# Kernel tuning notes

Hardware: AMD Instinct MI355X
Metric: run time of the kernel (lower is better)

Reference implementation:

```python
import jax, jax.numpy as jnp
import numpy as np

N_NODES, N_EDGES, D_IN, D_OUT = 50000, 400000, 512, 512


def setup_inputs() -> dict:
    key = jax.random.key(0)
    k = jax.random.split(key, 7)
    s = 1.0 / np.sqrt(D_IN)
    return {
        "x": jax.random.normal(k[0], (N_NODES, D_IN), dtype=jnp.float32),
        "src": jax.random.randint(k[1], (N_EDGES,), 0, N_NODES),
        "dst": jax.random.randint(k[2], (N_EDGES,), 0, N_NODES),
        "W1": jax.random.uniform(k[3], (D_IN, D_OUT), jnp.float32, -s, s),
        "b1": jax.random.uniform(k[4], (D_OUT,), jnp.float32, -s, s),
        "W2": jax.random.uniform(k[5], (D_IN, D_OUT), jnp.float32, -s, s),
        "b2": jax.random.uniform(k[6], (D_OUT,), jnp.float32, -s, s),
    }


def reference(x, src, dst, W1, b1, W2, b2):
    n_nodes = x.shape[0]
    # gather src features along each edge, segment-sum into dst nodes
    msg_sum = jax.ops.segment_sum(x[src], dst, num_segments=n_nodes)      # [N, D_in]
    counts = jax.ops.segment_sum(jnp.ones_like(dst, dtype=x.dtype), dst,
                                 num_segments=n_nodes)                    # [N]
    mean = msg_sum / jnp.maximum(counts, 1.0)[:, None]                    # mailbox mean
    out = (x @ W1 + b1) + ((x - mean) @ W2 + b2)
    # DGL update_all leaves nodes with no incoming messages untouched
    return jnp.where((counts > 0)[:, None], out, x)
```

## Files before the change

### kernel.cpp

```cpp
#include <hip/hip_runtime.h>
#include <hip/hip_bf16.h>
#include <stdint.h>

typedef unsigned short u16;
typedef unsigned int   u32;

#define N_NODES 50000
#define N_EDGES 400000
#define DDIM    512
#define KTOT    1024
#define BM      256
#define BMS     256
#define BN      256
#define BK      32
#define NT      (KTOT / BK)
#define MTILES  ((N_NODES + BM - 1) / BM)
#define NTILES  (DDIM / BN)
#define NWG     (MTILES * NTILES)

typedef __attribute__((ext_vector_type(8))) __bf16 bf16x8;
typedef __attribute__((ext_vector_type(4))) float  f32x4;

#define S_VMCNT(n) do { asm volatile("s_waitcnt vmcnt(" #n ")" ::: "memory"); \
                        __builtin_amdgcn_sched_barrier(0); } while (0)
#define S_LGKM0()  do { asm volatile("s_waitcnt lgkmcnt(0)" ::: "memory"); \
                        __builtin_amdgcn_sched_barrier(0); } while (0)

__device__ __forceinline__ float bflo(u32 d) { return __builtin_bit_cast(float, d << 16); }
__device__ __forceinline__ float bfhi(u32 d) { return __builtin_bit_cast(float, d & 0xffff0000u); }
__device__ __forceinline__ u16 f2bf(float f) {
    u32 u = __builtin_bit_cast(u32, f);
    u32 r = u + 0x7fffu + ((u >> 16) & 1u);
    return (u16)(r >> 16);
}
__device__ __forceinline__ u32 pack2(float a, float b) {
    return (u32)f2bf(a) | ((u32)f2bf(b) << 16);
}
__device__ __forceinline__ void gload_lds16(const void* g, void* l) {
    __builtin_amdgcn_global_load_lds(
        (const __attribute__((address_space(1))) void*)g,
        (__attribute__((address_space(3))) void*)l, 16, 0, 0);
}

__global__ void cvt_k(const float* __restrict__ x, u16* __restrict__ Acat) {
    int i = blockIdx.x * 256 + threadIdx.x;
    int node = i >> 6, c8 = i & 63;
    const float4* p = (const float4*)(x + (size_t)node * DDIM + c8 * 8);
    float4 a = p[0], b = p[1];
    uint4 o;
    o.x = pack2(a.x, a.y); o.y = pack2(a.z, a.w);
    o.z = pack2(b.x, b.y); o.w = pack2(b.z, b.w);
    *(uint4*)(Acat + (size_t)node * KTOT + c8 * 8) = o;
}

__global__ void hist_k(const int* __restrict__ dst, int* __restrict__ counts) {
    int e = blockIdx.x * 256 + threadIdx.x;
    if (e < N_EDGES) atomicAdd(&counts[dst[e]], 1);
}

#define NCHUNK 49
__global__ __launch_bounds__(1024) void scanA_k(const int* __restrict__ counts, int* __restrict__ csum) {
    __shared__ int ws[16];
    int t = threadIdx.x, b = blockIdx.x;
    int i = b * 1024 + t;
    int v = (i < N_NODES) ? counts[i] : 0;
    for (int d = 32; d; d >>= 1) v += __shfl_down(v, d);
    if ((t & 63) == 0) ws[t >> 6] = v;
    __syncthreads();
    if (t < 16) {
        int s = ws[t];
        for (int d = 8; d; d >>= 1) s += __shfl_down(s, d);
        if (t == 0) csum[b] = s;
    }
}
__global__ void scanB_k(int* __restrict__ csum) {
    int t = threadIdx.x;
    int v = (t < NCHUNK) ? csum[t] : 0;
    int s = v;
    for (int d = 1; d < 64; d <<= 1) { int u = __shfl_up(s, d); if (t >= d) s += u; }
    if (t < NCHUNK) csum[t] = s - v;
}
__global__ __launch_bounds__(1024) void scanC_k(const int* __restrict__ counts, const int* __restrict__ csum,
                                                int* __restrict__ offsets, int* __restrict__ cursor) {
    __shared__ int wsum[16];
    int t = threadIdx.x, b = blockIdx.x;
    int i = b * 1024 + t;
    int lane = t & 63, w = t >> 6;
    int v = (i < N_NODES) ? counts[i] : 0;
    int s = v;
    for (int d = 1; d < 64; d <<= 1) { int u = __shfl_up(s, d); if (lane >= d) s += u; }
    if (lane == 63) wsum[w] = s;
    __syncthreads();
    if (t < 16) {
        int ww = wsum[t], ss = ww;
        for (int d = 1; d < 16; d <<= 1) { int u = __shfl_up(ss, d); if (t >= d) ss += u; }
        wsum[t] = ss - ww;
    }
    __syncthreads();
    int excl = (s - v) + wsum[w] + csum[b];
    if (i < N_NODES) { offsets[i] = excl; cursor[i] = excl; }
}

__global__ void fill_k(const int* __restrict__ src, const int* __restrict__ dst,
                       int* __restrict__ cursor, int* __restrict__ esrc) {
    int e = blockIdx.x * 256 + threadIdx.x;
    if (e < N_EDGES) {
        int d = dst[e];
        int p = atomicAdd(&cursor[d], 1);
        esrc[p] = src[e];
    }
}

__global__ void prepw_k(const float* __restrict__ W1, const float* __restrict__ W2,
                        const float* __restrict__ b1, const float* __restrict__ b2,
                        u16* __restrict__ Wcat, float* __restrict__ b12) {
    int idx = blockIdx.x * 256 + threadIdx.x;
    int k = idx >> 9, n = idx & 511;
    float w1 = W1[idx], w2 = W2[idx];
    Wcat[(size_t)n * KTOT + k]       = f2bf(w1 + w2);
    Wcat[(size_t)n * KTOT + 512 + k] = f2bf(w2);
    if (idx < 512) b12[idx] = b1[idx] + b2[idx];
}

__device__ __forceinline__ void addrow(float* acc, uint4 v) {
    acc[0] += bflo(v.x); acc[1] += bfhi(v.x);
    acc[2] += bflo(v.y); acc[3] += bfhi(v.y);
    acc[4] += bflo(v.z); acc[5] += bfhi(v.z);
    acc[6] += bflo(v.w); acc[7] += bfhi(v.w);
}
__global__ __launch_bounds__(256) void agg_k(u16* Acat,
                                             const int* __restrict__ offsets,
                                             const int* __restrict__ counts,
                                             const int* __restrict__ esrc) {
    int nid = blockIdx.x * 4 + (threadIdx.x >> 6);
    if (nid >= N_NODES) return;
    int lane = threadIdx.x & 63;
    int off = offsets[nid], deg = counts[nid];
    float acc[8] = {0, 0, 0, 0, 0, 0, 0, 0};
    int e = 0;
    for (; e + 7 < deg; e += 8) {
        int s[8];
        #pragma unroll
        for (int u = 0; u < 8; u++) s[u] = esrc[off + e + u];
        uint4 v[8];
        #pragma unroll
        for (int u = 0; u < 8; u++)
            v[u] = *(const uint4*)(Acat + (size_t)s[u] * KTOT + lane * 8);
        #pragma unroll
        for (int u = 0; u < 8; u++) addrow(acc, v[u]);
    }
    for (; e + 3 < deg; e += 4) {
        int s0 = esrc[off + e], s1 = esrc[off + e + 1];
        int s2 = esrc[off + e + 2], s3 = esrc[off + e + 3];
        uint4 v0 = *(const uint4*)(Acat + (size_t)s0 * KTOT + lane * 8);
        uint4 v1 = *(const uint4*)(Acat + (size_t)s1 * KTOT + lane * 8);
        uint4 v2 = *(const uint4*)(Acat + (size_t)s2 * KTOT + lane * 8);
        uint4 v3 = *(const uint4*)(Acat + (size_t)s3 * KTOT + lane * 8);
        addrow(acc, v0); addrow(acc, v1); addrow(acc, v2); addrow(acc, v3);
    }
    for (; e < deg; e++) {
        int s0 = esrc[off + e];
        addrow(acc, *(const uint4*)(Acat + (size_t)s0 * KTOT + lane * 8));
    }
    float scale = (deg > 0) ? (-1.0f / (float)deg) : 0.0f;
    uint4 o;
    o.x = pack2(acc[0] * scale, acc[1] * scale);
    o.y = pack2(acc[2] * scale, acc[3] * scale);
    o.z = pack2(acc[4] * scale, acc[5] * scale);
    o.w = pack2(acc[6] * scale, acc[7] * scale);
    *(uint4*)(Acat + (size_t)nid * KTOT + 512 + lane * 8) = o;
}

__global__ __launch_bounds__(512, 2) void gemm_k(const u16* __restrict__ Acat,
                                                 const float* __restrict__ x,
                                                 const u16* __restrict__ Wcat,
                                                 const float* __restrict__ b12,
                                                 const int* __restrict__ counts,
                                                 float* __restrict__ out) {
    __shared__ u16 As[4][BMS * BK];
    __shared__ u16 Bs[4][BN * BK];

    const int tlin = (blockIdx.x & 7) * (NWG / 8) + (blockIdx.x >> 3);
    const int m0 = (tlin >> 1) * BM;
    const int n0 = (tlin & 1) * BN;

    const int tid  = threadIdx.x;
    const int lane = tid & 63;
    const int wid  = tid >> 6;
    const int wm = wid >> 2, wn = wid & 3;
    const int quad = lane >> 4, lr = lane & 15;

    const int rloc  = tid >> 2;
    const int koffu = (((tid & 3) ^ ((tid >> 3) & 3)) << 3);
    int arow[2], brow[2];
    #pragma unroll
    for (int q = 0; q < 2; q++) {
        int r = m0 + q * 128 + rloc;
        arow[q] = (r < N_NODES) ? r : (N_NODES - 1);
        brow[q] = n0 + q * 128 + rloc;
    }

    auto stage = [&](int t) {
        u16* A_c = &As[t & 3][0]; u16* B_c = &Bs[t & 3][0];
        const int k0 = t * BK;
        #pragma unroll
        for (int q = 0; q < 2; q++)
            gload_lds16(Acat + (size_t)arow[q] * KTOT + k0 + koffu,
                        A_c + q * 4096 + wid * 512);
        #pragma unroll
        for (int q = 0; q < 2; q++)
            gload_lds16(Wcat + (size_t)brow[q] * KTOT + k0 + koffu,
                        B_c + q * 4096 + wid * 512);
    };

    const int rswb = ((lr >> 1) & 3) << 4;
    auto ldA = [&](const u16* A_c, int mf) -> bf16x8 {
        int row = wm * 128 + mf * 16 + lr;
        return *(const bf16x8*)((const char*)A_c + row * 64 + ((quad << 4) ^ rswb));
    };
    auto ldB = [&](const u16* B_c, int nf) -> bf16x8 {
        int row = wn * 64 + nf * 16 + lr;
        return *(const bf16x8*)((const char*)B_c + row * 64 + ((quad << 4) ^ rswb));
    };

    f32x4 acc[8][4] = {};

    stage(0); stage(1); stage(2);
    S_VMCNT(8);
    __builtin_amdgcn_s_barrier();

    #pragma unroll 1
    for (int t = 0; t < NT; ++t) {
        const u16* A_c = &As[t & 3][0];
        const u16* B_c = &Bs[t & 3][0];

        bf16x8 af[8], bf[4];
        #pragma unroll
        for (int i = 0; i < 8; i++) af[i] = ldA(A_c, i);
        #pragma unroll
        for (int j = 0; j < 4; j++) bf[j] = ldB(B_c, j);

        if (t + 3 < NT) stage(t + 3);

        __builtin_amdgcn_s_setprio(1);
        #pragma unroll
        for (int i = 0; i < 8; i++)
            #pragma unroll
            for (int j = 0; j < 4; j++)
                acc[i][j] = __builtin_amdgcn_mfma_f32_16x16x32_bf16(af[i], bf[j], acc[i][j], 0, 0, 0);
        __builtin_amdgcn_s_setprio(0);

        S_LGKM0();
        if (t < NT - 3) {
            S_VMCNT(8);
            __builtin_amdgcn_s_barrier();
        } else if (t == NT - 3) {
            S_VMCNT(4);
            __builtin_amdgcn_s_barrier();
        } else if (t == NT - 2) {
            S_VMCNT(0);
            __builtin_amdgcn_s_barrier();
        }
    }

    #pragma unroll
    for (int i = 0; i < 8; i++) {
        #pragma unroll
        for (int r = 0; r < 4; r++) {
            int grow = m0 + wm * 128 + i * 16 + quad * 4 + r;
            if (grow >= N_NODES) continue;
            int cnt = counts[grow];
            #pragma unroll
            for (int j = 0; j < 4; j++) {
                int gcol = n0 + wn * 64 + j * 16 + lr;
                float v;
                if (cnt > 0) v = acc[i][j][r] + b12[gcol];
                else         v = x[(size_t)grow * DDIM + gcol];
                out[(size_t)grow * DDIM + gcol] = v;
            }
        }
    }
}

extern "C" void kernel_launch(void* const* d_in, const int* in_sizes, int n_in,
                              void* d_out, int out_size, void* d_ws, size_t ws_size,
                              hipStream_t stream) {
    const float* x  = (const float*)d_in[0];
    const int* src  = (const int*)d_in[1];
    const int* dst  = (const int*)d_in[2];
    const float* W1 = (const float*)d_in[3];
    const float* b1 = (const float*)d_in[4];
    const float* W2 = (const float*)d_in[5];
    const float* b2 = (const float*)d_in[6];
    float* out = (float*)d_out;

    char* ws = (char*)d_ws;
    size_t o = 0;
    auto alloc = [&](size_t bytes) { char* p = ws + o; o += (bytes + 255) & ~(size_t)255; return p; };
    int* counts   = (int*)alloc((size_t)N_NODES * 4);
    int* offsets  = (int*)alloc((size_t)N_NODES * 4);
    int* cursor   = (int*)alloc((size_t)N_NODES * 4);
    int* csum     = (int*)alloc((size_t)NCHUNK * 4);
    int* esrc     = (int*)alloc((size_t)N_EDGES * 4);
    u16* Wcat     = (u16*)alloc((size_t)512 * KTOT * 2);
    float* b12    = (float*)alloc((size_t)512 * 4);
    u16* Acat     = (u16*)alloc((size_t)N_NODES * KTOT * 2);
    (void)ws_size; (void)n_in; (void)in_sizes; (void)out_size;

    hipMemsetAsync(counts, 0, (size_t)N_NODES * 4, stream);
    cvt_k<<<(N_NODES * 64) / 256, 256, 0, stream>>>(x, Acat);
    hist_k<<<(N_EDGES + 255) / 256, 256, 0, stream>>>(dst, counts);
    scanA_k<<<NCHUNK, 1024, 0, stream>>>(counts, csum);
    scanB_k<<<1, 64, 0, stream>>>(csum);
    scanC_k<<<NCHUNK, 1024, 0, stream>>>(counts, csum, offsets, cursor);
    fill_k<<<(N_EDGES + 255) / 256, 256, 0, stream>>>(src, dst, cursor, esrc);
    prepw_k<<<(512 * 512) / 256, 256, 0, stream>>>(W1, W2, b1, b2, Wcat, b12);
    agg_k<<<(N_NODES + 3) / 4, 256, 0, stream>>>(Acat, offsets, counts, esrc);
    gemm_k<<<dim3(NWG), 512, 0, stream>>>(Acat, x, Wcat, b12, counts, out);
}
```

Before: 401.2 us.

## Load GEMM fragments directly from global memory with register double-buffering instead of LDS

The GEMM kernel no longer stages A and B tiles through shared memory with global_load_lds and barriers. Each wave now loads its MFMA fragments straight from global memory into registers, double-buffering two k-steps so one step's loads overlap the other step's MFMAs. This removes LDS traffic and the workgroup barriers. In exchange, operands shared across waves are fetched redundantly from global/L2 with 16-byte accesses strided by row, which raises memory traffic and register pressure.

```diff
diff --git a/kernel.cpp b/kernel.cpp
--- a/kernel.cpp
+++ b/kernel.cpp
@@ -10,7 +10,6 @@
 #define DDIM    512
 #define KTOT    1024
 #define BM      256
-#define BMS     256
 #define BN      256
 #define BK      32
 #define NT      (KTOT / BK)
@@ -23,8 +22,6 @@
 
 #define S_VMCNT(n) do { asm volatile("s_waitcnt vmcnt(" #n ")" ::: "memory"); \
                         __builtin_amdgcn_sched_barrier(0); } while (0)
-#define S_LGKM0()  do { asm volatile("s_waitcnt lgkmcnt(0)" ::: "memory"); \
-                        __builtin_amdgcn_sched_barrier(0); } while (0)
 
 __device__ __forceinline__ float bflo(u32 d) { return __builtin_bit_cast(float, d << 16); }
 __device__ __forceinline__ float bfhi(u32 d) { return __builtin_bit_cast(float, d & 0xffff0000u); }
@@ -35,11 +32,6 @@
 }
 __device__ __forceinline__ u32 pack2(float a, float b) {
     return (u32)f2bf(a) | ((u32)f2bf(b) << 16);
-}
-__device__ __forceinline__ void gload_lds16(const void* g, void* l) {
-    __builtin_amdgcn_global_load_lds(
-        (const __attribute__((address_space(1))) void*)g,
-        (__attribute__((address_space(3))) void*)l, 16, 0, 0);
 }
 
 __global__ void cvt_k(const float* __restrict__ x, u16* __restrict__ Acat) {
@@ -177,9 +169,6 @@
                                                  const float* __restrict__ b12,
                                                  const int* __restrict__ counts,
                                                  float* __restrict__ out) {
-    __shared__ u16 As[4][BMS * BK];
-    __shared__ u16 Bs[4][BN * BK];
-
     const int tlin = (blockIdx.x & 7) * (NWG / 8) + (blockIdx.x >> 3);
     const int m0 = (tlin >> 1) * BM;
     const int n0 = (tlin & 1) * BN;
@@ -190,77 +179,67 @@
     const int wm = wid >> 2, wn = wid & 3;
     const int quad = lane >> 4, lr = lane & 15;
 
-    const int rloc  = tid >> 2;
-    const int koffu = (((tid & 3) ^ ((tid >> 3) & 3)) << 3);
-    int arow[2], brow[2];
-    #pragma unroll
-    for (int q = 0; q < 2; q++) {
-        int r = m0 + q * 128 + rloc;
-        arow[q] = (r < N_NODES) ? r : (N_NODES - 1);
-        brow[q] = n0 + q * 128 + rloc;
-    }
-
-    auto stage = [&](int t) {
-        u16* A_c = &As[t & 3][0]; u16* B_c = &Bs[t & 3][0];
-        const int k0 = t * BK;
-        #pragma unroll
-        for (int q = 0; q < 2; q++)
-            gload_lds16(Acat + (size_t)arow[q] * KTOT + k0 + koffu,
-                        A_c + q * 4096 + wid * 512);
-        #pragma unroll
-        for (int q = 0; q < 2; q++)
-            gload_lds16(Wcat + (size_t)brow[q] * KTOT + k0 + koffu,
-                        B_c + q * 4096 + wid * 512);
-    };
-
-    const int rswb = ((lr >> 1) & 3) << 4;
-    auto ldA = [&](const u16* A_c, int mf) -> bf16x8 {
-        int row = wm * 128 + mf * 16 + lr;
-        return *(const bf16x8*)((const char*)A_c + row * 64 + ((quad << 4) ^ rswb));
-    };
-    auto ldB = [&](const u16* B_c, int nf) -> bf16x8 {
-        int row = wn * 64 + nf * 16 + lr;
-        return *(const bf16x8*)((const char*)B_c + row * 64 + ((quad << 4) ^ rswb));
-    };
+    u32 aoff[8], boff[4];
+    #pragma unroll
+    for (int i = 0; i < 8; i++) {
+        int r = m0 + wm * 128 + i * 16 + lr;
+        if (r > N_NODES - 1) r = N_NODES - 1;
+        aoff[i] = ((u32)r << 11) + (quad << 4);
+    }
+    #pragma unroll
+    for (int j = 0; j < 4; j++) {
+        int r = n0 + wn * 64 + j * 16 + lr;
+        boff[j] = ((u32)r << 11) + (quad << 4);
+    }
+
+    const char* Ab = (const char*)Acat;
+    const char* Bb = (const char*)Wcat;
 
     f32x4 acc[8][4] = {};
-
-    stage(0); stage(1); stage(2);
-    S_VMCNT(8);
-    __builtin_amdgcn_s_barrier();
+    bf16x8 afA[8], bfA[4], afB[8], bfB[4];
+
+    #pragma unroll
+    for (int i = 0; i < 8; i++) afA[i] = *(const bf16x8*)(Ab + aoff[i]);
+    #pragma unroll
+    for (int j = 0; j < 4; j++) bfA[j] = *(const bf16x8*)(Bb + boff[j]);
 
     #pragma unroll 1
-    for (int t = 0; t < NT; ++t) {
-        const u16* A_c = &As[t & 3][0];
-        const u16* B_c = &Bs[t & 3][0];
-
-        bf16x8 af[8], bf[4];
-        #pragma unroll
-        for (int i = 0; i < 8; i++) af[i] = ldA(A_c, i);
-        #pragma unroll
-        for (int j = 0; j < 4; j++) bf[j] = ldB(B_c, j);
-
-        if (t + 3 < NT) stage(t + 3);
-
+    for (int t = 0; t < NT; t += 2) {
+        {
+            const char* A1 = Ab + (size_t)(t + 1) * 64;
+            const char* B1 = Bb + (size_t)(t + 1) * 64;
+            #pragma unroll
+            for (int i = 0; i < 8; i++) afB[i] = *(const bf16x8*)(A1 + aoff[i]);
+            #pragma unroll
+            for (int j = 0; j < 4; j++) bfB[j] = *(const bf16x8*)(B1 + boff[j]);
+        }
+        S_VMCNT(12);
         __builtin_amdgcn_s_setprio(1);
         #pragma unroll
         for (int i = 0; i < 8; i++)
             #pragma unroll
             for (int j = 0; j < 4; j++)
-                acc[i][j] = __builtin_amdgcn_mfma_f32_16x16x32_bf16(af[i], bf[j], acc[i][j], 0, 0, 0);
+                acc[i][j] = __builtin_amdgcn_mfma_f32_16x16x32_bf16(afA[i], bfA[j], acc[i][j], 0, 0, 0);
         __builtin_amdgcn_s_setprio(0);
 
-        S_LGKM0();
-        if (t < NT - 3) {
-            S_VMCNT(8);
-            __builtin_amdgcn_s_barrier();
-        } else if (t == NT - 3) {
-            S_VMCNT(4);
-            __builtin_amdgcn_s_barrier();
-        } else if (t == NT - 2) {
+        if (t + 2 < NT) {
+            const char* A2 = Ab + (size_t)(t + 2) * 64;
+            const char* B2 = Bb + (size_t)(t + 2) * 64;
+            #pragma unroll
+            for (int i = 0; i < 8; i++) afA[i] = *(const bf16x8*)(A2 + aoff[i]);
+            #pragma unroll
+            for (int j = 0; j < 4; j++) bfA[j] = *(const bf16x8*)(B2 + boff[j]);
+            S_VMCNT(12);
+        } else {
             S_VMCNT(0);
-            __builtin_amdgcn_s_barrier();
         }
+        __builtin_amdgcn_s_setprio(1);
+        #pragma unroll
+        for (int i = 0; i < 8; i++)
+            #pragma unroll
+            for (int j = 0; j < 4; j++)
+                acc[i][j] = __builtin_amdgcn_mfma_f32_16x16x32_bf16(afB[i], bfB[j], acc[i][j], 0, 0, 0);
+        __builtin_amdgcn_s_setprio(0);
     }
 
     #pragma unroll
```

New measurement: 556.1 us. 1.39x slower.

## Fuse neighbor aggregation into GEMM prologue with full-width 128-row tiles

Applied to the files above, without the earlier changes.

Drops the separate aggregation kernel. Each GEMM workgroup now first gathers and averages neighbor features for its own 128 rows, writes them into the second half of Acat, then runs the GEMM. Tiles change from 256x256 to 128x512, so every workgroup covers the full output width and aggregation happens only once per row. This removes a kernel launch and lets the freshly written mean rows come back from cache. The cost is a serialized gather phase before the MFMA loop in every workgroup, plus occupancy cut to one workgroup per CU.

```diff
diff --git a/kernel.cpp b/kernel.cpp
--- a/kernel.cpp
+++ b/kernel.cpp
@@ -9,14 +9,11 @@
 #define N_EDGES 400000
 #define DDIM    512
 #define KTOT    1024
-#define BM      256
-#define BMS     256
-#define BN      256
+#define BM      128
+#define BN      512
 #define BK      32
 #define NT      (KTOT / BK)
 #define MTILES  ((N_NODES + BM - 1) / BM)
-#define NTILES  (DDIM / BN)
-#define NWG     (MTILES * NTILES)
 
 typedef __attribute__((ext_vector_type(8))) __bf16 bf16x8;
 typedef __attribute__((ext_vector_type(4))) float  f32x4;
@@ -128,105 +125,95 @@
     acc[4] += bflo(v.z); acc[5] += bfhi(v.z);
     acc[6] += bflo(v.w); acc[7] += bfhi(v.w);
 }
-__global__ __launch_bounds__(256) void agg_k(u16* Acat,
-                                             const int* __restrict__ offsets,
-                                             const int* __restrict__ counts,
-                                             const int* __restrict__ esrc) {
-    int nid = blockIdx.x * 4 + (threadIdx.x >> 6);
-    if (nid >= N_NODES) return;
-    int lane = threadIdx.x & 63;
-    int off = offsets[nid], deg = counts[nid];
-    float acc[8] = {0, 0, 0, 0, 0, 0, 0, 0};
-    int e = 0;
-    for (; e + 7 < deg; e += 8) {
-        int s[8];
-        #pragma unroll
-        for (int u = 0; u < 8; u++) s[u] = esrc[off + e + u];
-        uint4 v[8];
-        #pragma unroll
-        for (int u = 0; u < 8; u++)
-            v[u] = *(const uint4*)(Acat + (size_t)s[u] * KTOT + lane * 8);
-        #pragma unroll
-        for (int u = 0; u < 8; u++) addrow(acc, v[u]);
-    }
-    for (; e + 3 < deg; e += 4) {
-        int s0 = esrc[off + e], s1 = esrc[off + e + 1];
-        int s2 = esrc[off + e + 2], s3 = esrc[off + e + 3];
-        uint4 v0 = *(const uint4*)(Acat + (size_t)s0 * KTOT + lane * 8);
-        uint4 v1 = *(const uint4*)(Acat + (size_t)s1 * KTOT + lane * 8);
-        uint4 v2 = *(const uint4*)(Acat + (size_t)s2 * KTOT + lane * 8);
-        uint4 v3 = *(const uint4*)(Acat + (size_t)s3 * KTOT + lane * 8);
-        addrow(acc, v0); addrow(acc, v1); addrow(acc, v2); addrow(acc, v3);
-    }
-    for (; e < deg; e++) {
-        int s0 = esrc[off + e];
-        addrow(acc, *(const uint4*)(Acat + (size_t)s0 * KTOT + lane * 8));
-    }
-    float scale = (deg > 0) ? (-1.0f / (float)deg) : 0.0f;
-    uint4 o;
-    o.x = pack2(acc[0] * scale, acc[1] * scale);
-    o.y = pack2(acc[2] * scale, acc[3] * scale);
-    o.z = pack2(acc[4] * scale, acc[5] * scale);
-    o.w = pack2(acc[6] * scale, acc[7] * scale);
-    *(uint4*)(Acat + (size_t)nid * KTOT + 512 + lane * 8) = o;
-}
-
-__global__ __launch_bounds__(512, 2) void gemm_k(const u16* __restrict__ Acat,
+
+__global__ __launch_bounds__(512, 1) void gemm_k(u16* __restrict__ Acat,
                                                  const float* __restrict__ x,
                                                  const u16* __restrict__ Wcat,
                                                  const float* __restrict__ b12,
                                                  const int* __restrict__ counts,
+                                                 const int* __restrict__ offsets,
+                                                 const int* __restrict__ esrc,
                                                  float* __restrict__ out) {
-    __shared__ u16 As[4][BMS * BK];
+    __shared__ u16 As[4][BM * BK];
     __shared__ u16 Bs[4][BN * BK];
 
-    const int tlin = (blockIdx.x & 7) * (NWG / 8) + (blockIdx.x >> 3);
-    const int m0 = (tlin >> 1) * BM;
-    const int n0 = (tlin & 1) * BN;
-
+    const int m0 = blockIdx.x * BM;
     const int tid  = threadIdx.x;
     const int lane = tid & 63;
     const int wid  = tid >> 6;
     const int wm = wid >> 2, wn = wid & 3;
     const int quad = lane >> 4, lr = lane & 15;
 
+    #pragma unroll 1
+    for (int n = 0; n < 16; n++) {
+        int nid = m0 + wid * 16 + n;
+        if (nid >= N_NODES) break;
+        int off = offsets[nid], deg = counts[nid];
+        float acc8[8] = {0, 0, 0, 0, 0, 0, 0, 0};
+        int e = 0;
+        for (; e + 7 < deg; e += 8) {
+            int s[8];
+            #pragma unroll
+            for (int u = 0; u < 8; u++) s[u] = esrc[off + e + u];
+            uint4 v[8];
+            #pragma unroll
+            for (int u = 0; u < 8; u++)
+                v[u] = *(const uint4*)(Acat + (size_t)s[u] * KTOT + lane * 8);
+            #pragma unroll
+            for (int u = 0; u < 8; u++) addrow(acc8, v[u]);
+        }
+        for (; e + 3 < deg; e += 4) {
+            int s0 = esrc[off + e], s1 = esrc[off + e + 1];
+            int s2 = esrc[off + e + 2], s3 = esrc[off + e + 3];
+            uint4 v0 = *(const uint4*)(Acat + (size_t)s0 * KTOT + lane * 8);
+            uint4 v1 = *(const uint4*)(Acat + (size_t)s1 * KTOT + lane * 8);
+            uint4 v2 = *(const uint4*)(Acat + (size_t)s2 * KTOT + lane * 8);
+            uint4 v3 = *(const uint4*)(Acat + (size_t)s3 * KTOT + lane * 8);
+            addrow(acc8, v0); addrow(acc8, v1); addrow(acc8, v2); addrow(acc8, v3);
+        }
+        for (; e < deg; e++) {
+            int s0 = esrc[off + e];
+            addrow(acc8, *(const uint4*)(Acat + (size_t)s0 * KTOT + lane * 8));
+        }
+        float scale = (deg > 0) ? (-1.0f / (float)deg) : 0.0f;
+        uint4 o;
+        o.x = pack2(acc8[0] * scale, acc8[1] * scale);
+        o.y = pack2(acc8[2] * scale, acc8[3] * scale);
+        o.z = pack2(acc8[4] * scale, acc8[5] * scale);
+        o.w = pack2(acc8[6] * scale, acc8[7] * scale);
+        *(uint4*)(Acat + (size_t)nid * KTOT + 512 + lane * 8) = o;
+    }
+    __syncthreads();
+
     const int rloc  = tid >> 2;
     const int koffu = (((tid & 3) ^ ((tid >> 3) & 3)) << 3);
-    int arow[2], brow[2];
-    #pragma unroll
-    for (int q = 0; q < 2; q++) {
-        int r = m0 + q * 128 + rloc;
-        arow[q] = (r < N_NODES) ? r : (N_NODES - 1);
-        brow[q] = n0 + q * 128 + rloc;
-    }
+    int arow_c = m0 + rloc;
+    if (arow_c > N_NODES - 1) arow_c = N_NODES - 1;
 
     auto stage = [&](int t) {
         u16* A_c = &As[t & 3][0]; u16* B_c = &Bs[t & 3][0];
         const int k0 = t * BK;
-        #pragma unroll
-        for (int q = 0; q < 2; q++)
-            gload_lds16(Acat + (size_t)arow[q] * KTOT + k0 + koffu,
-                        A_c + q * 4096 + wid * 512);
-        #pragma unroll
-        for (int q = 0; q < 2; q++)
-            gload_lds16(Wcat + (size_t)brow[q] * KTOT + k0 + koffu,
+        gload_lds16(Acat + (size_t)arow_c * KTOT + k0 + koffu, A_c + wid * 512);
+        #pragma unroll
+        for (int q = 0; q < 4; q++)
+            gload_lds16(Wcat + (size_t)(q * 128 + rloc) * KTOT + k0 + koffu,
                         B_c + q * 4096 + wid * 512);
     };
 
     const int rswb = ((lr >> 1) & 3) << 4;
     auto ldA = [&](const u16* A_c, int mf) -> bf16x8 {
-        int row = wm * 128 + mf * 16 + lr;
+        int row = wm * 64 + mf * 16 + lr;
         return *(const bf16x8*)((const char*)A_c + row * 64 + ((quad << 4) ^ rswb));
     };
     auto ldB = [&](const u16* B_c, int nf) -> bf16x8 {
-        int row = wn * 64 + nf * 16 + lr;
+        int row = wn * 128 + nf * 16 + lr;
         return *(const bf16x8*)((const char*)B_c + row * 64 + ((quad << 4) ^ rswb));
     };
 
-    f32x4 acc[8][4] = {};
+    f32x4 acc[4][8] = {};
 
     stage(0); stage(1); stage(2);
-    S_VMCNT(8);
+    S_VMCNT(10);
     __builtin_amdgcn_s_barrier();
 
     #pragma unroll 1
@@ -234,28 +221,28 @@
         const u16* A_c = &As[t & 3][0];
         const u16* B_c = &Bs[t & 3][0];
 
-        bf16x8 af[8], bf[4];
-        #pragma unroll
-        for (int i = 0; i < 8; i++) af[i] = ldA(A_c, i);
-        #pragma unroll
-        for (int j = 0; j < 4; j++) bf[j] = ldB(B_c, j);
+        bf16x8 af[4], bf[8];
+        #pragma unroll
+        for (int i = 0; i < 4; i++) af[i] = ldA(A_c, i);
+        #pragma unroll
+        for (int j = 0; j < 8; j++) bf[j] = ldB(B_c, j);
 
         if (t + 3 < NT) stage(t + 3);
 
         __builtin_amdgcn_s_setprio(1);
         #pragma unroll
-        for (int i = 0; i < 8; i++)
-            #pragma unroll
-            for (int j = 0; j < 4; j++)
+        for (int i = 0; i < 4; i++)
+            #pragma unroll
+            for (int j = 0; j < 8; j++)
                 acc[i][j] = __builtin_amdgcn_mfma_f32_16x16x32_bf16(af[i], bf[j], acc[i][j], 0, 0, 0);
         __builtin_amdgcn_s_setprio(0);
 
         S_LGKM0();
         if (t < NT - 3) {
-            S_VMCNT(8);
+            S_VMCNT(10);
             __builtin_amdgcn_s_barrier();
         } else if (t == NT - 3) {
-            S_VMCNT(4);
+            S_VMCNT(5);
             __builtin_amdgcn_s_barrier();
         } else if (t == NT - 2) {
             S_VMCNT(0);
@@ -264,15 +251,15 @@
     }
 
     #pragma unroll
-    for (int i = 0; i < 8; i++) {
+    for (int i = 0; i < 4; i++) {
         #pragma unroll
         for (int r = 0; r < 4; r++) {
-            int grow = m0 + wm * 128 + i * 16 + quad * 4 + r;
+            int grow = m0 + wm * 64 + i * 16 + quad * 4 + r;
             if (grow >= N_NODES) continue;
             int cnt = counts[grow];
             #pragma unroll
-            for (int j = 0; j < 4; j++) {
-                int gcol = n0 + wn * 64 + j * 16 + lr;
+            for (int j = 0; j < 8; j++) {
+                int gcol = wn * 128 + j * 16 + lr;
                 float v;
                 if (cnt > 0) v = acc[i][j][r] + b12[gcol];
                 else         v = x[(size_t)grow * DDIM + gcol];
@@ -315,6 +302,5 @@
     scanC_k<<<NCHUNK, 1024, 0, stream>>>(counts, csum, offsets, cursor);
     fill_k<<<(N_EDGES + 255) / 256, 256, 0, stream>>>(src, dst, cursor, esrc);
     prepw_k<<<(512 * 512) / 256, 256, 0, stream>>>(W1, W2, b1, b2, Wcat, b12);
-    agg_k<<<(N_NODES + 3) / 4, 256, 0, stream>>>(Acat, offsets, counts, esrc);
-    gemm_k<<<dim3(NWG), 512, 0, stream>>>(Acat, x, Wcat, b12, counts, out);
-}
+    gemm_k<<<dim3(MTILES), 512, 0, stream>>>(Acat, x, Wcat, b12, counts, offsets, esrc, out);
+}
```

Result: slower. 427.0 us (+6.4%).

## Fuse prep kernels, single-block scan, split GEMM into two half launches

Applied to the files above, without the earlier changes.

Merges the bf16 conversion of x, the weight/bias preparation and the degree histogram into one launch, dispatched by block index. Replaces the three-kernel prefix scan with a single 1024-thread block that walks the 49 chunks serially with a running carry. Splits the GEMM into two launches over the two halves of the row tiles, with a remapped per-XCD block-to-tile assignment. The aim is to cut kernel-launch and dependency gaps, but the scan becomes serial and the GEMM split adds one launch and a tail per half.

```diff
diff --git a/kernel.cpp b/kernel.cpp
--- a/kernel.cpp
+++ b/kernel.cpp
@@ -10,13 +10,12 @@
 #define DDIM    512
 #define KTOT    1024
 #define BM      256
-#define BMS     256
 #define BN      256
 #define BK      32
 #define NT      (KTOT / BK)
 #define MTILES  ((N_NODES + BM - 1) / BM)
-#define NTILES  (DDIM / BN)
-#define NWG     (MTILES * NTILES)
+#define MHALF   (MTILES / 2)
+#define NWGH    (MHALF * 2)
 
 typedef __attribute__((ext_vector_type(8))) __bf16 bf16x8;
 typedef __attribute__((ext_vector_type(4))) float  f32x4;
@@ -42,63 +41,77 @@
         (__attribute__((address_space(3))) void*)l, 16, 0, 0);
 }
 
-__global__ void cvt_k(const float* __restrict__ x, u16* __restrict__ Acat) {
-    int i = blockIdx.x * 256 + threadIdx.x;
-    int node = i >> 6, c8 = i & 63;
-    const float4* p = (const float4*)(x + (size_t)node * DDIM + c8 * 8);
-    float4 a = p[0], b = p[1];
-    uint4 o;
-    o.x = pack2(a.x, a.y); o.y = pack2(a.z, a.w);
-    o.z = pack2(b.x, b.y); o.w = pack2(b.z, b.w);
-    *(uint4*)(Acat + (size_t)node * KTOT + c8 * 8) = o;
-}
-
-__global__ void hist_k(const int* __restrict__ dst, int* __restrict__ counts) {
-    int e = blockIdx.x * 256 + threadIdx.x;
-    if (e < N_EDGES) atomicAdd(&counts[dst[e]], 1);
+#define CVT_BLKS   ((N_NODES * 64) / 256)
+#define PREPW_BLKS ((512 * 512) / 256)
+#define HIST_BLKS  ((N_EDGES + 255) / 256)
+#define PREP_GRID  (CVT_BLKS + PREPW_BLKS + HIST_BLKS)
+
+__global__ __launch_bounds__(256) void prep_k(const float* __restrict__ x,
+                                              u16* __restrict__ Acat,
+                                              const float* __restrict__ W1,
+                                              const float* __restrict__ W2,
+                                              const float* __restrict__ b1,
+                                              const float* __restrict__ b2,
+                                              u16* __restrict__ Wcat,
+                                              float* __restrict__ b12,
+                                              const int* __restrict__ dst,
+                                              int* __restrict__ counts) {
+    int b = blockIdx.x;
+    if (b < CVT_BLKS) {
+        int i = b * 256 + threadIdx.x;
+        int node = i >> 6, c8 = i & 63;
+        const float4* p = (const float4*)(x + (size_t)node * DDIM + c8 * 8);
+        float4 a = p[0], bb = p[1];
+        uint4 o;
+        o.x = pack2(a.x, a.y);  o.y = pack2(a.z, a.w);
+        o.z = pack2(bb.x, bb.y); o.w = pack2(bb.z, bb.w);
+        *(uint4*)(Acat + (size_t)node * KTOT + c8 * 8) = o;
+    } else if (b < CVT_BLKS + PREPW_BLKS) {
+        int idx = (b - CVT_BLKS) * 256 + threadIdx.x;
+        int k = idx >> 9, n = idx & 511;
+        float w1 = W1[idx], w2 = W2[idx];
+        Wcat[(size_t)n * KTOT + k]       = f2bf(w1 + w2);
+        Wcat[(size_t)n * KTOT + 512 + k] = f2bf(w2);
+        if (idx < 512) b12[idx] = b1[idx] + b2[idx];
+    } else {
+        int e = (b - CVT_BLKS - PREPW_BLKS) * 256 + threadIdx.x;
+        if (e < N_EDGES) atomicAdd(&counts[dst[e]], 1);
+    }
 }
 
 #define NCHUNK 49
-__global__ __launch_bounds__(1024) void scanA_k(const int* __restrict__ counts, int* __restrict__ csum) {
-    __shared__ int ws[16];
-    int t = threadIdx.x, b = blockIdx.x;
-    int i = b * 1024 + t;
-    int v = (i < N_NODES) ? counts[i] : 0;
-    for (int d = 32; d; d >>= 1) v += __shfl_down(v, d);
-    if ((t & 63) == 0) ws[t >> 6] = v;
-    __syncthreads();
-    if (t < 16) {
-        int s = ws[t];
-        for (int d = 8; d; d >>= 1) s += __shfl_down(s, d);
-        if (t == 0) csum[b] = s;
-    }
-}
-__global__ void scanB_k(int* __restrict__ csum) {
+__global__ __launch_bounds__(1024) void scan_k(const int* __restrict__ counts,
+                                               int* __restrict__ offsets,
+                                               int* __restrict__ cursor) {
+    __shared__ int wsum[16];
+    __shared__ int tot;
+    __shared__ int carry;
     int t = threadIdx.x;
-    int v = (t < NCHUNK) ? csum[t] : 0;
-    int s = v;
-    for (int d = 1; d < 64; d <<= 1) { int u = __shfl_up(s, d); if (t >= d) s += u; }
-    if (t < NCHUNK) csum[t] = s - v;
-}
-__global__ __launch_bounds__(1024) void scanC_k(const int* __restrict__ counts, const int* __restrict__ csum,
-                                                int* __restrict__ offsets, int* __restrict__ cursor) {
-    __shared__ int wsum[16];
-    int t = threadIdx.x, b = blockIdx.x;
-    int i = b * 1024 + t;
     int lane = t & 63, w = t >> 6;
-    int v = (i < N_NODES) ? counts[i] : 0;
-    int s = v;
-    for (int d = 1; d < 64; d <<= 1) { int u = __shfl_up(s, d); if (lane >= d) s += u; }
-    if (lane == 63) wsum[w] = s;
-    __syncthreads();
-    if (t < 16) {
-        int ww = wsum[t], ss = ww;
-        for (int d = 1; d < 16; d <<= 1) { int u = __shfl_up(ss, d); if (t >= d) ss += u; }
-        wsum[t] = ss - ww;
-    }
-    __syncthreads();
-    int excl = (s - v) + wsum[w] + csum[b];
-    if (i < N_NODES) { offsets[i] = excl; cursor[i] = excl; }
+    if (t == 0) carry = 0;
+    int v = (t < N_NODES) ? counts[t] : 0;
+    #pragma unroll 1
+    for (int b = 0; b < NCHUNK; b++) {
+        int inext = (b + 1) * 1024 + t;
+        int vnext = (b + 1 < NCHUNK && inext < N_NODES) ? counts[inext] : 0;
+        int s = v;
+        for (int d = 1; d < 64; d <<= 1) { int u = __shfl_up(s, d); if (lane >= d) s += u; }
+        if (lane == 63) wsum[w] = s;
+        __syncthreads();
+        if (t < 16) {
+            int ww = wsum[t], ss = ww;
+            for (int d = 1; d < 16; d <<= 1) { int u = __shfl_up(ss, d); if (t >= d) ss += u; }
+            wsum[t] = ss - ww;
+            if (t == 15) tot = ss;
+        }
+        __syncthreads();
+        int i = b * 1024 + t;
+        int excl = (s - v) + wsum[w] + carry;
+        if (i < N_NODES) { offsets[i] = excl; cursor[i] = excl; }
+        __syncthreads();
+        if (t == 0) carry += tot;
+        v = vnext;
+    }
 }
 
 __global__ void fill_k(const int* __restrict__ src, const int* __restrict__ dst,
@@ -109,17 +122,6 @@
         int p = atomicAdd(&cursor[d], 1);
         esrc[p] = src[e];
     }
-}
-
-__global__ void prepw_k(const float* __restrict__ W1, const float* __restrict__ W2,
-                        const float* __restrict__ b1, const float* __restrict__ b2,
-                        u16* __restrict__ Wcat, float* __restrict__ b12) {
-    int idx = blockIdx.x * 256 + threadIdx.x;
-    int k = idx >> 9, n = idx & 511;
-    float w1 = W1[idx], w2 = W2[idx];
-    Wcat[(size_t)n * KTOT + k]       = f2bf(w1 + w2);
-    Wcat[(size_t)n * KTOT + 512 + k] = f2bf(w2);
-    if (idx < 512) b12[idx] = b1[idx] + b2[idx];
 }
 
 __device__ __forceinline__ void addrow(float* acc, uint4 v) {
@@ -176,13 +178,16 @@
                                                  const u16* __restrict__ Wcat,
                                                  const float* __restrict__ b12,
                                                  const int* __restrict__ counts,
-                                                 float* __restrict__ out) {
-    __shared__ u16 As[4][BMS * BK];
+                                                 float* __restrict__ out,
+                                                 int mbase) {
+    __shared__ u16 As[4][BM * BK];
     __shared__ u16 Bs[4][BN * BK];
 
-    const int tlin = (blockIdx.x & 7) * (NWG / 8) + (blockIdx.x >> 3);
-    const int m0 = (tlin >> 1) * BM;
-    const int n0 = (tlin & 1) * BN;
+    const int orig = blockIdx.x;
+    const int xcd = orig & 7, loc = orig >> 3;
+    const int wg = (xcd < 4 ? xcd * 25 : 100 + (xcd - 4) * 24) + loc;
+    const int m0 = mbase + (wg >> 1) * BM;
+    const int n0 = (wg & 1) * BN;
 
     const int tid  = threadIdx.x;
     const int lane = tid & 63;
@@ -300,7 +305,6 @@
     int* counts   = (int*)alloc((size_t)N_NODES * 4);
     int* offsets  = (int*)alloc((size_t)N_NODES * 4);
     int* cursor   = (int*)alloc((size_t)N_NODES * 4);
-    int* csum     = (int*)alloc((size_t)NCHUNK * 4);
     int* esrc     = (int*)alloc((size_t)N_EDGES * 4);
     u16* Wcat     = (u16*)alloc((size_t)512 * KTOT * 2);
     float* b12    = (float*)alloc((size_t)512 * 4);
@@ -308,13 +312,10 @@
     (void)ws_size; (void)n_in; (void)in_sizes; (void)out_size;
 
     hipMemsetAsync(counts, 0, (size_t)N_NODES * 4, stream);
-    cvt_k<<<(N_NODES * 64) / 256, 256, 0, stream>>>(x, Acat);
-    hist_k<<<(N_EDGES + 255) / 256, 256, 0, stream>>>(dst, counts);
-    scanA_k<<<NCHUNK, 1024, 0, stream>>>(counts, csum);
-    scanB_k<<<1, 64, 0, stream>>>(csum);
-    scanC_k<<<NCHUNK, 1024, 0, stream>>>(counts, csum, offsets, cursor);
-    fill_k<<<(N_EDGES + 255) / 256, 256, 0, stream>>>(src, dst, cursor, esrc);
-    prepw_k<<<(512 * 512) / 256, 256, 0, stream>>>(W1, W2, b1, b2, Wcat, b12);
+    prep_k<<<PREP_GRID, 256, 0, stream>>>(x, Acat, W1, W2, b1, b2, Wcat, b12, dst, counts);
+    scan_k<<<1, 1024, 0, stream>>>(counts, offsets, cursor);
+    fill_k<<<HIST_BLKS, 256, 0, stream>>>(src, dst, cursor, esrc);
     agg_k<<<(N_NODES + 3) / 4, 256, 0, stream>>>(Acat, offsets, counts, esrc);
-    gemm_k<<<dim3(NWG), 512, 0, stream>>>(Acat, x, Wcat, b12, counts, out);
-}
+    gemm_k<<<dim3(NWGH), 512, 0, stream>>>(Acat, x, Wcat, b12, counts, out, 0);
+    gemm_k<<<dim3(NWGH), 512, 0, stream>>>(Acat, x, Wcat, b12, counts, out, MHALF * BM);
+}
```

After: 437.5 us. +9.0%, slower.
